# Optimization experiments

Measured on AMD Instinct MI355X. Metric: run time of the kernel, lower is better.

The kernel has to match this reference:

```python
import jax, jax.numpy as jnp
import numpy as np

B, N, D, H = 4, 1024, 512, 8
DH = D // H  # per-head dim for V and for each of the two Q/K halves
LAM = 0.5


def setup_inputs() -> dict:
    key = jax.random.key(0)
    ks = jax.random.split(key, 7)
    s = 0.02
    return {
        "x": jax.random.normal(ks[0], (B, N, D), dtype=jnp.float32),
        "Wq": jax.random.normal(ks[1], (D, 2 * D), dtype=jnp.float32) * s,
        "bq": jax.random.normal(ks[2], (2 * D,), dtype=jnp.float32) * s,
        "Wk": jax.random.normal(ks[3], (D, 2 * D), dtype=jnp.float32) * s,
        "bk": jax.random.normal(ks[4], (2 * D,), dtype=jnp.float32) * s,
        "Wv": jax.random.normal(ks[5], (D, D), dtype=jnp.float32) * s,
        "bv": jax.random.normal(ks[6], (D,), dtype=jnp.float32) * s,
    }


def reference(x, Wq, bq, Wk, bk, Wv, bv):
    b, n, d = x.shape
    q = (x @ Wq + bq).reshape(b, n, H, 2 * DH).transpose(0, 2, 1, 3)  # [B,H,N,2*DH]
    k = (x @ Wk + bk).reshape(b, n, H, 2 * DH).transpose(0, 2, 1, 3)
    v = (x @ Wv + bv).reshape(b, n, H, DH).transpose(0, 2, 1, 3)      # [B,H,N,DH]
    q1, q2 = q[..., :DH], q[..., DH:]
    k1, k2 = k[..., :DH], k[..., DH:]
    scale = 1.0 / jnp.sqrt(jnp.float32(DH))
    a1 = jax.nn.softmax(jnp.einsum("bhqd,bhkd->bhqk", q1, k1) * scale, axis=-1)
    a2 = jax.nn.softmax(jnp.einsum("bhqd,bhkd->bhqk", q2, k2) * scale, axis=-1)
    attn = a1 - LAM * a2                                              # [B,H,N,N]
    out = jnp.einsum("bhqk,bhkd->bhqd", attn, v)                      # [B,H,N,DH]
    return out.transpose(0, 2, 1, 3).reshape(b, n, d)
```

## Files before the change

kernel.cpp:

```cpp
#include <hip/hip_runtime.h>
#include <hip/hip_bf16.h>

typedef unsigned short u16;
typedef unsigned int u32;
typedef short s16x8 __attribute__((ext_vector_type(8)));
typedef short s16x4 __attribute__((ext_vector_type(4)));
typedef float f32x4 __attribute__((ext_vector_type(4)));
typedef float f32x16 __attribute__((ext_vector_type(16)));

__device__ inline u16 f2bf(float f) {
  union { float f; unsigned int u; } v; v.f = f;
  unsigned int r = v.u + 0x7fffu + ((v.u >> 16) & 1u);
  return (u16)(r >> 16);
}

__device__ __forceinline__ u32 cvt_pk_bf16(float lo, float hi) {
  u32 r;
  asm("v_cvt_pk_bf16_f32 %0, %1, %2" : "=v"(r) : "v"(lo), "v"(hi));
  return r;
}

__device__ __forceinline__ void g2lds16(const u16* g, u16* l) {
  __builtin_amdgcn_global_load_lds((const __attribute__((address_space(1))) void*)g,
                                   (__attribute__((address_space(3))) void*)l, 16, 0, 0);
}

__global__ __launch_bounds__(256) void prep_kernel(const float* __restrict__ x, u16* __restrict__ xb,
                                                   const float* __restrict__ Wq,
                                                   const float* __restrict__ Wk,
                                                   const float* __restrict__ Wv,
                                                   u16* __restrict__ wt) {
  if (blockIdx.x >= 40) {
    int i = (((blockIdx.x - 40) * 8 + blockIdx.y) * 256 + threadIdx.x) * 8;
    float4 a = *(const float4*)(x + i);
    float4 b = *(const float4*)(x + i + 4);
    s16x8 o;
    o[0] = (short)f2bf(a.x); o[1] = (short)f2bf(a.y);
    o[2] = (short)f2bf(a.z); o[3] = (short)f2bf(a.w);
    o[4] = (short)f2bf(b.x); o[5] = (short)f2bf(b.y);
    o[6] = (short)f2bf(b.z); o[7] = (short)f2bf(b.w);
    *(s16x8*)(xb + i) = o;
    return;
  }
  __shared__ float tile[64][65];
  int jg = blockIdx.x * 64;
  const float* src; int C, j0;
  if (jg < 1024)      { src = Wq; C = 1024; j0 = jg; }
  else if (jg < 2048) { src = Wk; C = 1024; j0 = jg - 1024; }
  else                { src = Wv; C = 512;  j0 = jg - 2048; }
  int k0 = blockIdx.y * 64;
  int tx = threadIdx.x % 64, ty4 = threadIdx.x / 64;
#pragma unroll
  for (int p = 0; p < 16; ++p) {
    int r = p * 4 + ty4;
    tile[r][tx] = src[(size_t)(k0 + r) * C + j0 + tx];
  }
  __syncthreads();
#pragma unroll
  for (int p = 0; p < 16; ++p) {
    int r = p * 4 + ty4;
    wt[(size_t)(jg + r) * 512 + k0 + tx] = f2bf(tile[tx][r]);
  }
}

__global__ __launch_bounds__(256, 2) void gemm_qkv(const u16* __restrict__ xb, const u16* __restrict__ wt,
                                                   const float* __restrict__ bq, const float* __restrict__ bk,
                                                   const float* __restrict__ bv,
                                                   u16* __restrict__ qa, u16* __restrict__ ka,
                                                   u16* __restrict__ va) {
  __shared__ __align__(16) u16 As[128 * 64];
  __shared__ __align__(16) u16 Bs[128 * 64];
  int m0 = blockIdx.x * 128, j0 = blockIdx.y * 128;
  bool isV = (j0 >= 2048);
  int tid = threadIdx.x;
  int w = tid >> 6, lane = tid & 63, quad = lane >> 4, l16 = lane & 15;
  int wr = (w >> 1) * 64, wc = (w & 1) * 64;

  int srow[4], scol[4], sbase[4];
#pragma unroll
  for (int it = 0; it < 4; ++it) {
    int s = it * 256 + tid;
    srow[it] = s >> 3;
    scol[it] = (s & 7) ^ ((s >> 3) & 7);
    sbase[it] = (s & ~63) * 8;
  }

  f32x4 acc[4][4];
#pragma unroll
  for (int i = 0; i < 4; ++i)
#pragma unroll
    for (int j = 0; j < 4; ++j)
#pragma unroll
      for (int r = 0; r < 4; ++r) acc[i][j][r] = 0.f;

  for (int kk = 0; kk < 8; ++kk) {
    int k0 = kk * 64;
    __syncthreads();
#pragma unroll
    for (int it = 0; it < 4; ++it) {
      g2lds16(xb + (size_t)(m0 + srow[it]) * 512 + k0 + scol[it] * 8, &As[sbase[it]]);
      g2lds16(wt + (size_t)(j0 + srow[it]) * 512 + k0 + scol[it] * 8, &Bs[sbase[it]]);
    }
    __syncthreads();
#pragma unroll
    for (int kb = 0; kb < 2; ++kb) {
      s16x8 af[4], bfr[4];
#pragma unroll
      for (int rb = 0; rb < 4; ++rb) {
        int row = wr + rb * 16 + l16;
        af[rb] = *(const s16x8*)(&As[row * 64 + (((kb * 4 + quad) ^ (row & 7)) * 8)]);
      }
#pragma unroll
      for (int cb = 0; cb < 4; ++cb) {
        int row = wc + cb * 16 + l16;
        bfr[cb] = *(const s16x8*)(&Bs[row * 64 + (((kb * 4 + quad) ^ (row & 7)) * 8)]);
      }
      if (isV) {
#pragma unroll
        for (int rb = 0; rb < 4; ++rb)
#pragma unroll
          for (int cb = 0; cb < 4; ++cb)
            acc[rb][cb] = __builtin_amdgcn_mfma_f32_16x16x32_bf16(bfr[cb], af[rb], acc[rb][cb], 0, 0, 0);
      } else {
#pragma unroll
        for (int rb = 0; rb < 4; ++rb)
#pragma unroll
          for (int cb = 0; cb < 4; ++cb)
            acc[rb][cb] = __builtin_amdgcn_mfma_f32_16x16x32_bf16(af[rb], bfr[cb], acc[rb][cb], 0, 0, 0);
      }
    }
  }

  if (isV) {
#pragma unroll
    for (int cb = 0; cb < 4; ++cb) {
#pragma unroll
      for (int rb = 0; rb < 4; ++rb) {
        int m = m0 + wr + rb * 16 + l16;
        int bidx = m >> 10, n = m & 1023;
#pragma unroll
        for (int r = 0; r < 4; ++r) {
          int jj = j0 - 2048 + wc + cb * 16 + quad * 4 + r;
          int h = jj >> 6, d = jj & 63;
          float bias = bv[jj];
          va[((size_t)((bidx * 8 + h) * 64 + d)) * 1024 + n] = f2bf(acc[rb][cb][r] + bias);
        }
      }
    }
  } else {
#pragma unroll
    for (int cb = 0; cb < 4; ++cb) {
      int j = j0 + wc + cb * 16 + l16;
      float bias = (j < 1024) ? bq[j] : bk[j - 1024];
#pragma unroll
      for (int rb = 0; rb < 4; ++rb) {
#pragma unroll
        for (int r = 0; r < 4; ++r) {
          int m = m0 + wr + rb * 16 + quad * 4 + r;
          int bidx = m >> 10, n = m & 1023;
          u16 o = f2bf(acc[rb][cb][r] + bias);
          if (j < 1024) {
            int h = j >> 7, r2 = j & 127;
            qa[((size_t)((bidx * 8 + h) * 1024 + n)) * 128 + r2] = o;
          } else {
            int jj = j - 1024, h = jj >> 7, r2 = jj & 127;
            ka[((size_t)((bidx * 8 + h) * 1024 + n)) * 128 + r2] = o;
          }
        }
      }
    }
  }
}

__global__ __launch_bounds__(256, 2) void attn_kernel(const u16* __restrict__ qa, const u16* __restrict__ ka,
                                                      const u16* __restrict__ va, float* __restrict__ out) {
  __shared__ __align__(16) u16 smem[40960];
  int bh = blockIdx.x, b = bh >> 3, h = bh & 7;
  int q0 = blockIdx.y * 64;
  int tid = threadIdx.x, w = tid >> 6, lane = tid & 63;
  int l32 = lane & 31, hi = lane >> 5;
  int team = w >> 1, wq = w & 1, t = tid & 127;
  u16* hb = smem + team * 20480;
  u16* const KbA = hb;
  u16* const KbB = hb + 8192;
  u16* const Vsb = hb + 16384;

  const u16* qrow = qa + (size_t)(bh * 1024 + q0 + wq * 32 + l32) * 128;
  s16x8 qf[2][4];
#pragma unroll
  for (int hh = 0; hh < 2; ++hh)
#pragma unroll
    for (int kb = 0; kb < 4; ++kb)
      qf[hh][kb] = *(const s16x8*)(qrow + 64 * hh + 16 * kb + 8 * hi);

  f32x16 O1[2], O2[2];
#pragma unroll
  for (int d = 0; d < 2; ++d)
#pragma unroll
    for (int r = 0; r < 16; ++r) { O1[d][r] = 0.f; O2[d][r] = 0.f; }
  float ds1 = 0.f, ds2 = 0.f;

  int r0 = t >> 4, c0 = t & 15;
  int rv = t >> 3, cv = (t & 7) ^ ((t >> 3) & 7);
  const u16* kgbase = ka + (size_t)bh * 1024 * 128;
  const u16* vgbase = va + (size_t)bh * 64 * 1024;
  int nbase = team * 512;

  auto stageK = [&](int n0, u16* Kd) {
#pragma unroll
    for (int it = 0; it < 8; ++it) {
      int row = r0 + 8 * it;
      int chunk = c0 ^ (row & 15);
      g2lds16(kgbase + (size_t)(n0 + row) * 128 + chunk * 8, Kd + (it * 128 + (t & 64)) * 8);
    }
  };
  auto stageV = [&](int n0) {
#pragma unroll
    for (int it = 0; it < 4; ++it)
      g2lds16(vgbase + (size_t)(rv + 16 * it) * 1024 + n0 + cv * 8, Vsb + (it * 128 + (t & 64)) * 8);
  };

  stageK(nbase, KbA);
  stageV(nbase);
  __syncthreads();

  for (int kt = 0; kt < 8; ++kt) {
    u16* const KsC = (kt & 1) ? KbB : KbA;
    u16* const KsN = (kt & 1) ? KbA : KbB;
    if (kt < 7) stageK(nbase + (kt + 1) * 64, KsN);

    s16x8 pa[2][4];
#pragma unroll
    for (int hh = 0; hh < 2; ++hh) {
      f32x16 sv[2];
#pragma unroll
      for (int nb = 0; nb < 2; ++nb)
#pragma unroll
        for (int r = 0; r < 16; ++r) sv[nb][r] = 0.f;
#pragma unroll
      for (int nb = 0; nb < 2; ++nb) {
        int row = nb * 32 + l32, rbase = row * 128, rx15 = row & 15;
#pragma unroll
        for (int kb = 0; kb < 4; ++kb) {
          s16x8 kf = *(const s16x8*)(&KsC[rbase + (((8 * hh + 2 * kb + hi) ^ rx15) * 8)]);
          sv[nb] = __builtin_amdgcn_mfma_f32_32x32x16_bf16(kf, qf[hh][kb], sv[nb], 0, 0, 0);
        }
      }
      float dsl = 0.f;
#pragma unroll
      for (int s = 0; s < 4; ++s) {
        float e[8];
#pragma unroll
        for (int j = 0; j < 8; ++j) {
          e[j] = __builtin_exp2f(sv[s >> 1][(s & 1) * 8 + j] * 0.18033688f);
          dsl += e[j];
        }
        union { u32 wd[4]; s16x8 v; } u;
        u.wd[0] = cvt_pk_bf16(e[0], e[1]);
        u.wd[1] = cvt_pk_bf16(e[2], e[3]);
        u.wd[2] = cvt_pk_bf16(e[4], e[5]);
        u.wd[3] = cvt_pk_bf16(e[6], e[7]);
        pa[hh][s] = u.v;
      }
      if (hh == 0) ds1 += dsl; else ds2 += dsl;
    }

    s16x8 vB[4][2];
#pragma unroll
    for (int dblk = 0; dblk < 2; ++dblk) {
      int row = dblk * 32 + l32, rbase = row * 64, rx = row & 7;
#pragma unroll
      for (int s = 0; s < 4; ++s) {
        union { s16x4 hl[2]; s16x8 v; } u;
        u.hl[0] = *(const s16x4*)(&Vsb[rbase + (((2 * s) ^ rx) * 8) + 4 * hi]);
        u.hl[1] = *(const s16x4*)(&Vsb[rbase + (((2 * s + 1) ^ rx) * 8) + 4 * hi]);
        vB[s][dblk] = u.v;
      }
    }

    asm volatile("s_waitcnt lgkmcnt(0)\n\ts_barrier" ::: "memory");
    if (kt < 7) stageV(nbase + (kt + 1) * 64);

#pragma unroll
    for (int s = 0; s < 4; ++s)
#pragma unroll
      for (int dblk = 0; dblk < 2; ++dblk) {
        O1[dblk] = __builtin_amdgcn_mfma_f32_32x32x16_bf16(pa[0][s], vB[s][dblk], O1[dblk], 0, 0, 0);
        O2[dblk] = __builtin_amdgcn_mfma_f32_32x32x16_bf16(pa[1][s], vB[s][dblk], O2[dblk], 0, 0, 0);
      }

    __syncthreads();
  }

  float* scr = (float*)smem;
  int mbase = wq * 4224 + lane;
  if (team == 1) {
#pragma unroll
    for (int r = 0; r < 16; ++r) {
      scr[mbase + r * 64]        = O1[0][r];
      scr[mbase + (16 + r) * 64] = O1[1][r];
      scr[mbase + (32 + r) * 64] = O2[0][r];
      scr[mbase + (48 + r) * 64] = O2[1][r];
    }
    scr[mbase + 64 * 64] = ds1;
    scr[mbase + 65 * 64] = ds2;
  }
  __syncthreads();
  if (team == 0) {
#pragma unroll
    for (int r = 0; r < 16; ++r) {
      O1[0][r] += scr[mbase + r * 64];
      O1[1][r] += scr[mbase + (16 + r) * 64];
      O2[0][r] += scr[mbase + (32 + r) * 64];
      O2[1][r] += scr[mbase + (48 + r) * 64];
    }
    ds1 += scr[mbase + 64 * 64];
    ds2 += scr[mbase + 65 * 64];
    ds1 += __shfl_xor(ds1, 32, 64);
    ds2 += __shfl_xor(ds2, 32, 64);
    float inv1 = 1.0f / ds1, inv2 = 1.0f / ds2;
#pragma unroll
    for (int r = 0; r < 16; ++r) {
      int iq = (r & 3) + 8 * (r >> 2) + 4 * hi;
      float i1 = __shfl(inv1, iq, 64);
      float i2 = __shfl(inv2, iq, 64);
      size_t orow = (size_t)(b * 1024 + q0 + wq * 32 + iq) * 512 + h * 64 + l32;
      out[orow]      = O1[0][r] * i1 - 0.5f * O2[0][r] * i2;
      out[orow + 32] = O1[1][r] * i1 - 0.5f * O2[1][r] * i2;
    }
  }
}

extern "C" void kernel_launch(void* const* d_in, const int* in_sizes, int n_in,
                              void* d_out, int out_size, void* d_ws, size_t ws_size,
                              hipStream_t stream) {
  (void)in_sizes; (void)n_in; (void)out_size; (void)ws_size;
  const float* x  = (const float*)d_in[0];
  const float* Wq = (const float*)d_in[1];
  const float* bq = (const float*)d_in[2];
  const float* Wk = (const float*)d_in[3];
  const float* bk = (const float*)d_in[4];
  const float* Wv = (const float*)d_in[5];
  const float* bv = (const float*)d_in[6];
  float* out = (float*)d_out;

  char* ws = (char*)d_ws;
  u16* xb = (u16*)(ws);
  u16* wt = (u16*)(ws + 4194304);
  u16* qa = (u16*)(ws + 6815744);
  u16* ka = (u16*)(ws + 15204352);
  u16* va = (u16*)(ws + 23592960);

  prep_kernel<<<dim3(168, 8), 256, 0, stream>>>(x, xb, Wq, Wk, Wv, wt);
  gemm_qkv<<<dim3(32, 20), 256, 0, stream>>>(xb, wt, bq, bk, bv, qa, ka, va);
  attn_kernel<<<dim3(32, 16), 256, 0, stream>>>(qa, ka, va, out);
}
```

Before: 132.5 us.

## Fold softmax scale into Q projection and restructure attention loop with precomputed offsets

Folds the softmax scale (log2e/sqrt(dh)) into the Q projection epilogue so the attention inner loop drops one multiply per score. The attention main loop is unrolled by two with a lambda body, which removes the runtime buffer selection. LDS read offsets and global prefetch pointers are precomputed once and advanced incrementally instead of being recomputed each iteration. V fragment LDS reads are moved ahead of the QK MFMAs to overlap LDS latency, and the row-sum uses a tree reduction. This raises register pressure from the offset and pointer arrays, which may hurt occupancy at launch bounds of 2, and rounding Q to bf16 after scaling slightly changes numerics.

```diff
diff --git a/kernel.cpp b/kernel.cpp
--- a/kernel.cpp
+++ b/kernel.cpp
@@ -151,15 +151,17 @@
 #pragma unroll
     for (int cb = 0; cb < 4; ++cb) {
       int j = j0 + wc + cb * 16 + l16;
-      float bias = (j < 1024) ? bq[j] : bk[j - 1024];
+      bool isQ = (j < 1024);
+      float bias = isQ ? bq[j] : bk[j - 1024];
 #pragma unroll
       for (int rb = 0; rb < 4; ++rb) {
 #pragma unroll
         for (int r = 0; r < 4; ++r) {
           int m = m0 + wr + rb * 16 + quad * 4 + r;
           int bidx = m >> 10, n = m & 1023;
-          u16 o = f2bf(acc[rb][cb][r] + bias);
-          if (j < 1024) {
+          float val = acc[rb][cb][r] + bias;
+          u16 o = f2bf(isQ ? val * 0.18033688f : val);
+          if (isQ) {
             int h = j >> 7, r2 = j & 127;
             qa[((size_t)((bidx * 8 + h) * 1024 + n)) * 128 + r2] = o;
           } else {
@@ -200,36 +202,72 @@
     for (int r = 0; r < 16; ++r) { O1[d][r] = 0.f; O2[d][r] = 0.f; }
   float ds1 = 0.f, ds2 = 0.f;
 
-  int r0 = t >> 4, c0 = t & 15;
-  int rv = t >> 3, cv = (t & 7) ^ ((t >> 3) & 7);
+  int ko[2][2][4];
+#pragma unroll
+  for (int nb = 0; nb < 2; ++nb) {
+    int row = nb * 32 + l32, rb = row * 128, rx = row & 15;
+#pragma unroll
+    for (int hh = 0; hh < 2; ++hh)
+#pragma unroll
+      for (int kb = 0; kb < 4; ++kb)
+        ko[nb][hh][kb] = rb + (((8 * hh + 2 * kb + hi) ^ rx) * 8);
+  }
+  int vo[2][4][2];
+#pragma unroll
+  for (int dblk = 0; dblk < 2; ++dblk) {
+    int row = dblk * 32 + l32, rb = row * 64, rx = row & 7;
+#pragma unroll
+    for (int s = 0; s < 4; ++s)
+#pragma unroll
+      for (int half = 0; half < 2; ++half)
+        vo[dblk][s][half] = rb + (((2 * s + half) ^ rx) * 8) + 4 * hi;
+  }
+
+  int nbase = team * 512;
   const u16* kgbase = ka + (size_t)bh * 1024 * 128;
   const u16* vgbase = va + (size_t)bh * 64 * 1024;
-  int nbase = team * 512;
-
-  auto stageK = [&](int n0, u16* Kd) {
-#pragma unroll
-    for (int it = 0; it < 8; ++it) {
-      int row = r0 + 8 * it;
-      int chunk = c0 ^ (row & 15);
-      g2lds16(kgbase + (size_t)(n0 + row) * 128 + chunk * 8, Kd + (it * 128 + (t & 64)) * 8);
-    }
-  };
-  auto stageV = [&](int n0) {
-#pragma unroll
-    for (int it = 0; it < 4; ++it)
-      g2lds16(vgbase + (size_t)(rv + 16 * it) * 1024 + n0 + cv * 8, Vsb + (it * 128 + (t & 64)) * 8);
-  };
-
-  stageK(nbase, KbA);
-  stageV(nbase);
+  int r0 = t >> 4, c0 = t & 15;
+  int ce = c0 ^ r0, co = c0 ^ (r0 + 8);
+  const u16* kp[8];
+#pragma unroll
+  for (int i2 = 0; i2 < 4; ++i2) {
+    kp[2 * i2]     = kgbase + (size_t)(nbase + r0 + 16 * i2) * 128 + ce * 8;
+    kp[2 * i2 + 1] = kgbase + (size_t)(nbase + r0 + 16 * i2 + 8) * 128 + co * 8;
+  }
+  int rv = t >> 3, cv = (t & 7) ^ ((t >> 3) & 7);
+  const u16* vp[4];
+#pragma unroll
+  for (int it = 0; it < 4; ++it)
+    vp[it] = vgbase + (size_t)(rv + 16 * it) * 1024 + nbase + cv * 8;
+  int dk[8];
+#pragma unroll
+  for (int it = 0; it < 8; ++it) dk[it] = (it * 128 + (t & 64)) * 8;
+
+#pragma unroll
+  for (int it = 0; it < 8; ++it) g2lds16(kp[it], KbA + dk[it]);
+#pragma unroll
+  for (int it = 0; it < 4; ++it) g2lds16(vp[it], Vsb + dk[it]);
   __syncthreads();
 
-  for (int kt = 0; kt < 8; ++kt) {
-    u16* const KsC = (kt & 1) ? KbB : KbA;
-    u16* const KsN = (kt & 1) ? KbA : KbB;
-    if (kt < 7) stageK(nbase + (kt + 1) * 64, KsN);
-
-    s16x8 pa[2][4];
+  s16x8 pa[2][4];
+  s16x8 vB[4][2];
+
+  auto body = [&](u16* const cur, u16* const nxt, bool pfK, bool pfV) {
+    if (pfK) {
+#pragma unroll
+      for (int it = 0; it < 8; ++it) kp[it] += 64 * 128;
+#pragma unroll
+      for (int it = 0; it < 8; ++it) g2lds16(kp[it], nxt + dk[it]);
+    }
+#pragma unroll
+    for (int dblk = 0; dblk < 2; ++dblk)
+#pragma unroll
+      for (int s = 0; s < 4; ++s) {
+        union { s16x4 hl[2]; s16x8 v; } u;
+        u.hl[0] = *(const s16x4*)(Vsb + vo[dblk][s][0]);
+        u.hl[1] = *(const s16x4*)(Vsb + vo[dblk][s][1]);
+        vB[s][dblk] = u.v;
+      }
 #pragma unroll
     for (int hh = 0; hh < 2; ++hh) {
       f32x16 sv[2];
@@ -238,23 +276,20 @@
 #pragma unroll
         for (int r = 0; r < 16; ++r) sv[nb][r] = 0.f;
 #pragma unroll
-      for (int nb = 0; nb < 2; ++nb) {
-        int row = nb * 32 + l32, rbase = row * 128, rx15 = row & 15;
+      for (int nb = 0; nb < 2; ++nb)
 #pragma unroll
         for (int kb = 0; kb < 4; ++kb) {
-          s16x8 kf = *(const s16x8*)(&KsC[rbase + (((8 * hh + 2 * kb + hi) ^ rx15) * 8)]);
+          s16x8 kf = *(const s16x8*)(cur + ko[nb][hh][kb]);
           sv[nb] = __builtin_amdgcn_mfma_f32_32x32x16_bf16(kf, qf[hh][kb], sv[nb], 0, 0, 0);
         }
-      }
       float dsl = 0.f;
 #pragma unroll
       for (int s = 0; s < 4; ++s) {
         float e[8];
 #pragma unroll
-        for (int j = 0; j < 8; ++j) {
-          e[j] = __builtin_exp2f(sv[s >> 1][(s & 1) * 8 + j] * 0.18033688f);
-          dsl += e[j];
-        }
+        for (int j = 0; j < 8; ++j)
+          e[j] = __builtin_exp2f(sv[s >> 1][(s & 1) * 8 + j]);
+        dsl += ((e[0] + e[1]) + (e[2] + e[3])) + ((e[4] + e[5]) + (e[6] + e[7]));
         union { u32 wd[4]; s16x8 v; } u;
         u.wd[0] = cvt_pk_bf16(e[0], e[1]);
         u.wd[1] = cvt_pk_bf16(e[2], e[3]);
@@ -264,23 +299,13 @@
       }
       if (hh == 0) ds1 += dsl; else ds2 += dsl;
     }
-
-    s16x8 vB[4][2];
-#pragma unroll
-    for (int dblk = 0; dblk < 2; ++dblk) {
-      int row = dblk * 32 + l32, rbase = row * 64, rx = row & 7;
-#pragma unroll
-      for (int s = 0; s < 4; ++s) {
-        union { s16x4 hl[2]; s16x8 v; } u;
-        u.hl[0] = *(const s16x4*)(&Vsb[rbase + (((2 * s) ^ rx) * 8) + 4 * hi]);
-        u.hl[1] = *(const s16x4*)(&Vsb[rbase + (((2 * s + 1) ^ rx) * 8) + 4 * hi]);
-        vB[s][dblk] = u.v;
-      }
-    }
-
     asm volatile("s_waitcnt lgkmcnt(0)\n\ts_barrier" ::: "memory");
-    if (kt < 7) stageV(nbase + (kt + 1) * 64);
-
+    if (pfV) {
+#pragma unroll
+      for (int it = 0; it < 4; ++it) vp[it] += 64;
+#pragma unroll
+      for (int it = 0; it < 4; ++it) g2lds16(vp[it], Vsb + dk[it]);
+    }
 #pragma unroll
     for (int s = 0; s < 4; ++s)
 #pragma unroll
@@ -288,8 +313,12 @@
         O1[dblk] = __builtin_amdgcn_mfma_f32_32x32x16_bf16(pa[0][s], vB[s][dblk], O1[dblk], 0, 0, 0);
         O2[dblk] = __builtin_amdgcn_mfma_f32_32x32x16_bf16(pa[1][s], vB[s][dblk], O2[dblk], 0, 0, 0);
       }
-
     __syncthreads();
+  };
+
+  for (int kt2 = 0; kt2 < 4; ++kt2) {
+    body(KbA, KbB, true, true);
+    body(KbB, KbA, kt2 < 3, kt2 < 3);
   }
 
   float* scr = (float*)smem;
```

Result: slower. 180.5 us (+36.2%).
